# Kernel optimization log

Measured on AMD Instinct MI355X. Metric: run time of the kernel, lower is better.

The kernel has to match this reference:

```python
import jax, jax.numpy as jnp
import numpy as np

B, L, H, Q = 64, 512, 1024, 64
VA_H = 256


def setup_inputs() -> dict:
    key = jax.random.key(0)
    ks = jax.random.split(key, 10)
    hidden_states = jax.random.normal(ks[0], (B, L, H), dtype=jnp.float32)
    quad_spans = jax.random.randint(ks[1], (B, Q, 4), 0, L, dtype=jnp.int64)
    quad_mask = jnp.ones((B, Q), dtype=jnp.int32)
    s = 0.02
    W1 = jax.random.normal(ks[2], (3 * H, VA_H), dtype=jnp.float32) * s
    b1 = jnp.zeros((VA_H,), dtype=jnp.float32)
    W2 = jax.random.normal(ks[3], (VA_H, VA_H // 2), dtype=jnp.float32) * s
    b2 = jnp.zeros((VA_H // 2,), dtype=jnp.float32)
    W3 = jax.random.normal(ks[4], (VA_H // 2, 2), dtype=jnp.float32) * s
    b3 = jnp.zeros((2,), dtype=jnp.float32)
    return {"hidden_states": hidden_states, "quad_spans": quad_spans,
            "quad_mask": quad_mask, "W1": W1, "b1": b1, "W2": W2, "b2": b2,
            "W3": W3, "b3": b3}


def _pool_spans(hidden_states, quad_spans, quad_mask):
    # hidden_states [B,L,H]; quad_spans [B,Q,4]; quad_mask [B,Q]
    Bn, Ln, Hn = hidden_states.shape
    pos = jnp.arange(Ln)[None, None, :]                      # [1,1,L]
    asp_s = quad_spans[:, :, 0:1]
    asp_e = quad_spans[:, :, 1:2]
    opi_s = quad_spans[:, :, 2:3]
    opi_e = quad_spans[:, :, 3:4]
    asp_valid = asp_s >= 2
    opi_valid = opi_s >= 2
    sep = pos == 1                                           # [SEP] fallback
    asp_m = ((pos >= asp_s) & (pos <= asp_e) & asp_valid) | (~asp_valid & sep)
    opi_m = ((pos >= opi_s) & (pos <= opi_e) & opi_valid) | (~opi_valid & sep)
    qm = (quad_mask != 0)[:, :, None]
    asp_f = (asp_m & qm).astype(hidden_states.dtype)         # [B,Q,L]
    opi_f = (opi_m & qm).astype(hidden_states.dtype)
    h_asp = jnp.einsum('bql,blh->bqh', asp_f, hidden_states) / jnp.clip(
        asp_f.sum(-1, keepdims=True), 1.0, None)
    h_opi = jnp.einsum('bql,blh->bqh', opi_f, hidden_states) / jnp.clip(
        opi_f.sum(-1, keepdims=True), 1.0, None)
    return h_asp, h_opi


def reference(hidden_states, quad_spans, quad_mask, W1, b1, W2, b2, W3, b3):
    h_asp, h_opi = _pool_spans(hidden_states, quad_spans, quad_mask)
    h_pair = jnp.concatenate([h_asp, h_opi, h_asp * h_opi], axis=-1)  # [B,Q,3H]
    x = jax.nn.gelu(h_pair @ W1 + b1, approximate=False)   # torch GELU = exact
    x = jax.nn.gelu(x @ W2 + b2, approximate=False)        # dropout: eval mode
    x = x @ W3 + b3                                        # [B,Q,2]
    va = jax.nn.sigmoid(x) * 8.0 + 1.0
    return va * quad_mask[:, :, None].astype(va.dtype)
```

## Files before the change

kernel.cpp:

```cpp
#include <hip/hip_runtime.h>
#include <math.h>


typedef __attribute__((ext_vector_type(4))) float f32x4;
typedef __attribute__((ext_vector_type(8))) short bf16x8;

#define NPAIR 4096
#define LSEQ 512
#define HDIM 1024

__device__ __forceinline__ unsigned short f2bf(float f) {
  unsigned int x = __float_as_uint(f);
  return (unsigned short)((x + 0x7fffu + ((x >> 16) & 1u)) >> 16);
}
__device__ __forceinline__ unsigned int pack2(float lo, float hi) {
  return (unsigned int)f2bf(lo) | ((unsigned int)f2bf(hi) << 16);
}

__global__ __launch_bounds__(256, 2) void pool_mfma_kernel(
    const float* __restrict__ hs, const int* __restrict__ spans,
    const int* __restrict__ qmask, unsigned short* __restrict__ hpair) {
  __shared__ __align__(16) unsigned short Bl[128][40];
  __shared__ float S[128][129];
  __shared__ float scl[128];

  const int b = blockIdx.x >> 3;
  const int n0 = (blockIdx.x & 7) * 128;
  const int tid = threadIdx.x;
  const int lane = tid & 63;
  const int lm = lane & 15, quad = lane >> 4;
  const int wm = (tid >> 6) * 32;

  const bool is64 =
      (spans[1] == 0) && (spans[3] == 0) && (spans[5] == 0) && (spans[7] == 0);

  auto span_of = [&](int r, int& s, int& e) {
    const int q = r & 63, t = r >> 6;
    const int idx = (b * 64 + q) * 4 + t * 2;
    s = is64 ? spans[idx * 2] : spans[idx];
    e = is64 ? spans[idx * 2 + 2] : spans[idx + 1];
    if (s < 2) { s = 1; e = 1; }
  };
  int s0, e0, s1, e1;
  span_of(wm + lm, s0, e0);
  span_of(wm + 16 + lm, s1, e1);

  if (tid < 128) {
    int s, e;
    span_of(tid, s, e);
    const int c = (e >= s) ? (e - s + 1) : 0;
    const float sc = 1.f / (float)(c < 1 ? 1 : c);
    scl[tid] = (qmask[b * 64 + (tid & 63)] != 0) ? sc : 0.f;
  }

  f32x4 acc[2][8];
#pragma unroll
  for (int f = 0; f < 2; ++f)
#pragma unroll
    for (int g = 0; g < 8; ++g) acc[f][g] = f32x4{0.f, 0.f, 0.f, 0.f};

  const float* hsb = hs + (size_t)b * (LSEQ * HDIM);
  const int nl = tid & 127;
  const int kb = (tid >> 7) * 16;

  for (int k0 = 0; k0 < LSEQ; k0 += 32) {
    const float* src = hsb + (size_t)(k0 + kb) * HDIM + n0 + nl;
    unsigned int tmp[8];
#pragma unroll
    for (int i = 0; i < 8; ++i) {
      const float f0 = src[(size_t)(2 * i) * HDIM];
      const float f1 = src[(size_t)(2 * i + 1) * HDIM];
      tmp[i] = pack2(f0, f1);
    }
    __syncthreads();
    *(uint4*)&Bl[nl][kb] = make_uint4(tmp[0], tmp[1], tmp[2], tmp[3]);
    *(uint4*)&Bl[nl][kb + 8] = make_uint4(tmp[4], tmp[5], tmp[6], tmp[7]);
    __syncthreads();

    bf16x8 a0, a1;
#pragma unroll
    for (int j = 0; j < 8; ++j) {
      const int k = k0 + quad * 8 + j;
      a0[j] = (short)((k >= s0 && k <= e0) ? 0x3F80 : 0);
      a1[j] = (short)((k >= s1 && k <= e1) ? 0x3F80 : 0);
    }
#pragma unroll
    for (int g = 0; g < 8; ++g) {
      bf16x8 bg = *(const bf16x8*)&Bl[g * 16 + lm][quad * 8];
      acc[0][g] = __builtin_amdgcn_mfma_f32_16x16x32_bf16(a0, bg, acc[0][g], 0, 0, 0);
      acc[1][g] = __builtin_amdgcn_mfma_f32_16x16x32_bf16(a1, bg, acc[1][g], 0, 0, 0);
    }
  }

#pragma unroll
  for (int f = 0; f < 2; ++f)
#pragma unroll
    for (int g = 0; g < 8; ++g)
#pragma unroll
      for (int r = 0; r < 4; ++r)
        S[wm + f * 16 + quad * 4 + r][g * 16 + lm] = acc[f][g][r];
  __syncthreads();

  const int q = tid >> 2;
  const int cg = (tid & 3) * 32;
  const float sA = scl[q], sO = scl[64 + q];
  unsigned short* dst = hpair + (size_t)(b * 64 + q) * 3072 + n0 + cg;
#pragma unroll
  for (int j4 = 0; j4 < 4; ++j4) {
    float a[8], o[8];
#pragma unroll
    for (int i = 0; i < 8; ++i) {
      a[i] = S[q][cg + j4 * 8 + i] * sA;
      o[i] = S[64 + q][cg + j4 * 8 + i] * sO;
    }
    uint4 wa, wo, wp;
    wa.x = pack2(a[0], a[1]); wa.y = pack2(a[2], a[3]);
    wa.z = pack2(a[4], a[5]); wa.w = pack2(a[6], a[7]);
    wo.x = pack2(o[0], o[1]); wo.y = pack2(o[2], o[3]);
    wo.z = pack2(o[4], o[5]); wo.w = pack2(o[6], o[7]);
    wp.x = pack2(a[0] * o[0], a[1] * o[1]); wp.y = pack2(a[2] * o[2], a[3] * o[3]);
    wp.z = pack2(a[4] * o[4], a[5] * o[5]); wp.w = pack2(a[6] * o[6], a[7] * o[7]);
    *(uint4*)(dst + j4 * 8) = wa;
    *(uint4*)(dst + 1024 + j4 * 8) = wo;
    *(uint4*)(dst + 2048 + j4 * 8) = wp;
  }
}

__global__ void transpose_f32_bf16(const float* __restrict__ in,
                                   unsigned short* __restrict__ out, int R,
                                   int C) {
  __shared__ float t[32][33];
  const int c0 = blockIdx.x * 32, r0 = blockIdx.y * 32;
  const int x = threadIdx.x, y = threadIdx.y;
#pragma unroll
  for (int i = 0; i < 32; i += 8)
    if (r0 + y + i < R && c0 + x < C)
      t[y + i][x] = in[(size_t)(r0 + y + i) * C + c0 + x];
  __syncthreads();
#pragma unroll
  for (int i = 0; i < 32; i += 8)
    if (c0 + y + i < C && r0 + x < R)
      out[(size_t)(c0 + y + i) * R + r0 + x] = f2bf(t[x][y + i]);
}

template <int ACT>
__global__ __launch_bounds__(256) void gemm_bt_bias_act(
    const unsigned short* __restrict__ A, const unsigned short* __restrict__ Bt,
    const float* __restrict__ bias, unsigned short* __restrict__ C, int M,
    int N, int K) {
  __shared__ __align__(16) unsigned short Al[64][40];
  __shared__ __align__(16) unsigned short Bl[64][40];
  const int bm = blockIdx.x * 64, bn = blockIdx.y * 64;
  const int tid = threadIdx.x;
  const int wave = tid >> 6, lane = tid & 63;
  const int wm = (wave & 1) * 32, wn = (wave >> 1) * 32;
  const int ar = tid >> 2, ac = (tid & 3) * 8;
  const int lm = lane & 15, lk = (lane >> 4) * 8;

  f32x4 acc00 = {0.f, 0.f, 0.f, 0.f}, acc01 = {0.f, 0.f, 0.f, 0.f};
  f32x4 acc10 = {0.f, 0.f, 0.f, 0.f}, acc11 = {0.f, 0.f, 0.f, 0.f};

  const unsigned short* pa = A + (size_t)(bm + ar) * K + ac;
  const unsigned short* pb = Bt + (size_t)(bn + ar) * K + ac;

  for (int k0 = 0; k0 < K; k0 += 32) {
    uint4 va = *(const uint4*)(pa + k0);
    uint4 vb = *(const uint4*)(pb + k0);
    *(uint4*)&Al[ar][ac] = va;
    *(uint4*)&Bl[ar][ac] = vb;
    __syncthreads();
    bf16x8 a0 = *(const bf16x8*)&Al[wm + lm][lk];
    bf16x8 a1 = *(const bf16x8*)&Al[wm + 16 + lm][lk];
    bf16x8 b0 = *(const bf16x8*)&Bl[wn + lm][lk];
    bf16x8 b1 = *(const bf16x8*)&Bl[wn + 16 + lm][lk];
    acc00 = __builtin_amdgcn_mfma_f32_16x16x32_bf16(a0, b0, acc00, 0, 0, 0);
    acc01 = __builtin_amdgcn_mfma_f32_16x16x32_bf16(a0, b1, acc01, 0, 0, 0);
    acc10 = __builtin_amdgcn_mfma_f32_16x16x32_bf16(a1, b0, acc10, 0, 0, 0);
    acc11 = __builtin_amdgcn_mfma_f32_16x16x32_bf16(a1, b1, acc11, 0, 0, 0);
    __syncthreads();
  }

  const int r0 = bm + wm + ((lane >> 4) << 2);
  const int c0 = bn + wn + lm;
  const float bs0 = bias[c0];
  const float bs1 = bias[c0 + 16];
  auto emit = [&](f32x4 v, int row0, int col, float bs) {
#pragma unroll
    for (int r = 0; r < 4; ++r) {
      float x = v[r] + bs;
      if (ACT == 1) x = 0.5f * x * (1.f + erff(x * 0.70710678118654752f));
      C[(size_t)(row0 + r) * N + col] = f2bf(x);
    }
  };
  emit(acc00, r0, c0, bs0);
  emit(acc10, r0 + 16, c0, bs0);
  emit(acc01, r0, c0 + 16, bs1);
  emit(acc11, r0 + 16, c0 + 16, bs1);
}

__global__ __launch_bounds__(256) void head_kernel(
    const unsigned short* __restrict__ x2, const float* __restrict__ W3,
    const float* __restrict__ b3, const int* __restrict__ qmask,
    float* __restrict__ out) {
  __shared__ float w3[256];
  const int tid = threadIdx.x;
  w3[tid] = W3[tid];
  __syncthreads();
  const int p = blockIdx.x * 256 + tid;
  float acc0 = b3[0];
  float acc1 = b3[1];
  const uint4* xr = (const uint4*)(x2 + (size_t)p * 128);
#pragma unroll
  for (int kk = 0; kk < 16; ++kk) {
    uint4 v = xr[kk];
    const int k = kk * 8;
    float x0 = __uint_as_float((v.x & 0xffffu) << 16);
    float x1 = __uint_as_float((v.x >> 16) << 16);
    float x2e = __uint_as_float((v.y & 0xffffu) << 16);
    float x3 = __uint_as_float((v.y >> 16) << 16);
    float x4 = __uint_as_float((v.z & 0xffffu) << 16);
    float x5 = __uint_as_float((v.z >> 16) << 16);
    float x6 = __uint_as_float((v.w & 0xffffu) << 16);
    float x7 = __uint_as_float((v.w >> 16) << 16);
    acc0 += x0 * w3[2 * k + 0];  acc1 += x0 * w3[2 * k + 1];
    acc0 += x1 * w3[2 * k + 2];  acc1 += x1 * w3[2 * k + 3];
    acc0 += x2e * w3[2 * k + 4]; acc1 += x2e * w3[2 * k + 5];
    acc0 += x3 * w3[2 * k + 6];  acc1 += x3 * w3[2 * k + 7];
    acc0 += x4 * w3[2 * k + 8];  acc1 += x4 * w3[2 * k + 9];
    acc0 += x5 * w3[2 * k + 10]; acc1 += x5 * w3[2 * k + 11];
    acc0 += x6 * w3[2 * k + 12]; acc1 += x6 * w3[2 * k + 13];
    acc0 += x7 * w3[2 * k + 14]; acc1 += x7 * w3[2 * k + 15];
  }
  const float qmf = (float)qmask[p];
  const float v0 = (1.f / (1.f + expf(-acc0))) * 8.f + 1.f;
  const float v1 = (1.f / (1.f + expf(-acc1))) * 8.f + 1.f;
  out[p * 2 + 0] = v0 * qmf;
  out[p * 2 + 1] = v1 * qmf;
}

extern "C" void kernel_launch(void* const* d_in, const int* in_sizes, int n_in,
                              void* d_out, int out_size, void* d_ws,
                              size_t ws_size, hipStream_t stream) {
  const float* hs = (const float*)d_in[0];
  const int* spans = (const int*)d_in[1];
  const int* qmask = (const int*)d_in[2];
  const float* W1 = (const float*)d_in[3];
  const float* b1 = (const float*)d_in[4];
  const float* W2 = (const float*)d_in[5];
  const float* b2 = (const float*)d_in[6];
  const float* W3 = (const float*)d_in[7];
  const float* b3 = (const float*)d_in[8];
  float* out = (float*)d_out;

  const size_t HPAIR_B = 25165824;
  const size_t X1_B = 2097152, X2_B = 1048576;
  const size_t W1T_B = 1572864;

  char* ws = (char*)d_ws;
  size_t off = 0;
  unsigned short* hpair = (unsigned short*)(ws + off); off += HPAIR_B;
  unsigned short* x1 = (unsigned short*)(ws + off);    off += X1_B;
  unsigned short* x2 = (unsigned short*)(ws + off);    off += X2_B;
  unsigned short* W1T = (unsigned short*)(ws + off);   off += W1T_B;
  unsigned short* W2T = (unsigned short*)(ws + off);

  transpose_f32_bf16<<<dim3(8, 96), dim3(32, 8), 0, stream>>>(W1, W1T, 3072,
                                                              256);
  transpose_f32_bf16<<<dim3(4, 8), dim3(32, 8), 0, stream>>>(W2, W2T, 256,
                                                             128);
  pool_mfma_kernel<<<512, 256, 0, stream>>>(hs, spans, qmask, hpair);
  gemm_bt_bias_act<1><<<dim3(64, 4), 256, 0, stream>>>(hpair, W1T, b1, x1,
                                                       NPAIR, 256, 3072);
  gemm_bt_bias_act<1><<<dim3(64, 2), 256, 0, stream>>>(x1, W2T, b2, x2, NPAIR,
                                                       128, 256);
  head_kernel<<<16, 256, 0, stream>>>(x2, W3, b3, qmask, out);
}
```

Measured before the change: 267.4 us.

## Double-buffer pooling loads, split-K GEMM1, fuse GEMM2 with head, merge transposes

The pooling kernel now double-buffers its LDS tile, using a shared buffer that is reused for the output staging. This lets the global loads for the next K chunk overlap the MFMA work on the current one. GEMM1 is split along K into two halves to double the grid from 256 blocks, followed by a separate reduce+bias+GELU kernel. GEMM2 is fused with the final 128->2 head so x2 is no longer written out, and the two weight transposes are merged into one launch. The split-K path adds an extra fp32 partial-buffer round trip and one more kernel launch.

```diff
diff --git a/kernel.cpp b/kernel.cpp
--- a/kernel.cpp
+++ b/kernel.cpp
@@ -16,13 +16,18 @@
 __device__ __forceinline__ unsigned int pack2(float lo, float hi) {
   return (unsigned int)f2bf(lo) | ((unsigned int)f2bf(hi) << 16);
 }
+__device__ __forceinline__ float gelu(float x) {
+  return 0.5f * x * (1.f + erff(x * 0.70710678118654752f));
+}
 
 __global__ __launch_bounds__(256, 2) void pool_mfma_kernel(
     const float* __restrict__ hs, const int* __restrict__ spans,
     const int* __restrict__ qmask, unsigned short* __restrict__ hpair) {
-  __shared__ __align__(16) unsigned short Bl[128][40];
-  __shared__ float S[128][129];
+  __shared__ __align__(16) unsigned char smem[66048];
   __shared__ float scl[128];
+  typedef unsigned short BlT[128][40];
+  BlT* Bl = (BlT*)smem;
+  float(*S)[129] = (float(*)[129])smem;
 
   const int b = blockIdx.x >> 3;
   const int n0 = (blockIdx.x & 7) * 128;
@@ -63,19 +68,25 @@
   const int nl = tid & 127;
   const int kb = (tid >> 7) * 16;
 
-  for (int k0 = 0; k0 < LSEQ; k0 += 32) {
-    const float* src = hsb + (size_t)(k0 + kb) * HDIM + n0 + nl;
-    unsigned int tmp[8];
+  auto load16 = [&](int kbase, unsigned int (&tmp)[8]) {
+    const float* src = hsb + (size_t)(kbase + kb) * HDIM + n0 + nl;
 #pragma unroll
     for (int i = 0; i < 8; ++i) {
       const float f0 = src[(size_t)(2 * i) * HDIM];
       const float f1 = src[(size_t)(2 * i + 1) * HDIM];
       tmp[i] = pack2(f0, f1);
     }
-    __syncthreads();
-    *(uint4*)&Bl[nl][kb] = make_uint4(tmp[0], tmp[1], tmp[2], tmp[3]);
-    *(uint4*)&Bl[nl][kb + 8] = make_uint4(tmp[4], tmp[5], tmp[6], tmp[7]);
-    __syncthreads();
+  };
+
+  unsigned int tmp[8];
+  load16(0, tmp);
+  *(uint4*)&Bl[0][nl][kb] = make_uint4(tmp[0], tmp[1], tmp[2], tmp[3]);
+  *(uint4*)&Bl[0][nl][kb + 8] = make_uint4(tmp[4], tmp[5], tmp[6], tmp[7]);
+
+  for (int it = 0; it < 16; ++it) {
+    const int k0 = it * 32;
+    __syncthreads();
+    if (it < 15) load16(k0 + 32, tmp);
 
     bf16x8 a0, a1;
 #pragma unroll
@@ -84,14 +95,21 @@
       a0[j] = (short)((k >= s0 && k <= e0) ? 0x3F80 : 0);
       a1[j] = (short)((k >= s1 && k <= e1) ? 0x3F80 : 0);
     }
+    const BlT& Bc = Bl[it & 1];
 #pragma unroll
     for (int g = 0; g < 8; ++g) {
-      bf16x8 bg = *(const bf16x8*)&Bl[g * 16 + lm][quad * 8];
+      bf16x8 bg = *(const bf16x8*)&Bc[g * 16 + lm][quad * 8];
       acc[0][g] = __builtin_amdgcn_mfma_f32_16x16x32_bf16(a0, bg, acc[0][g], 0, 0, 0);
       acc[1][g] = __builtin_amdgcn_mfma_f32_16x16x32_bf16(a1, bg, acc[1][g], 0, 0, 0);
     }
-  }
-
+    if (it < 15) {
+      BlT& Bn = Bl[(it + 1) & 1];
+      *(uint4*)&Bn[nl][kb] = make_uint4(tmp[0], tmp[1], tmp[2], tmp[3]);
+      *(uint4*)&Bn[nl][kb + 8] = make_uint4(tmp[4], tmp[5], tmp[6], tmp[7]);
+    }
+  }
+
+  __syncthreads();
 #pragma unroll
   for (int f = 0; f < 2; ++f)
 #pragma unroll
@@ -126,31 +144,40 @@
   }
 }
 
-__global__ void transpose_f32_bf16(const float* __restrict__ in,
-                                   unsigned short* __restrict__ out, int R,
-                                   int C) {
+__global__ void transpose_two(const float* __restrict__ W1,
+                              unsigned short* __restrict__ W1T,
+                              const float* __restrict__ W2,
+                              unsigned short* __restrict__ W2T) {
   __shared__ float t[32][33];
-  const int c0 = blockIdx.x * 32, r0 = blockIdx.y * 32;
+  const float* in;
+  unsigned short* out;
+  int R, C, c0, r0;
+  int blk = blockIdx.x;
+  if (blk < 768) {
+    in = W1; out = W1T; R = 3072; C = 256;
+    c0 = (blk & 7) * 32; r0 = (blk >> 3) * 32;
+  } else {
+    blk -= 768;
+    in = W2; out = W2T; R = 256; C = 128;
+    c0 = (blk & 3) * 32; r0 = (blk >> 2) * 32;
+  }
   const int x = threadIdx.x, y = threadIdx.y;
 #pragma unroll
   for (int i = 0; i < 32; i += 8)
-    if (r0 + y + i < R && c0 + x < C)
-      t[y + i][x] = in[(size_t)(r0 + y + i) * C + c0 + x];
+    t[y + i][x] = in[(size_t)(r0 + y + i) * C + c0 + x];
   __syncthreads();
 #pragma unroll
   for (int i = 0; i < 32; i += 8)
-    if (c0 + y + i < C && r0 + x < R)
-      out[(size_t)(c0 + y + i) * R + r0 + x] = f2bf(t[x][y + i]);
-}
-
-template <int ACT>
-__global__ __launch_bounds__(256) void gemm_bt_bias_act(
+    out[(size_t)(c0 + y + i) * R + r0 + x] = f2bf(t[x][y + i]);
+}
+
+__global__ __launch_bounds__(256) void gemm_bt_partial(
     const unsigned short* __restrict__ A, const unsigned short* __restrict__ Bt,
-    const float* __restrict__ bias, unsigned short* __restrict__ C, int M,
-    int N, int K) {
+    float* __restrict__ P, int M, int N, int K, int KH) {
   __shared__ __align__(16) unsigned short Al[64][40];
   __shared__ __align__(16) unsigned short Bl[64][40];
   const int bm = blockIdx.x * 64, bn = blockIdx.y * 64;
+  const int kz = blockIdx.z * KH;
   const int tid = threadIdx.x;
   const int wave = tid >> 6, lane = tid & 63;
   const int wm = (wave & 1) * 32, wn = (wave >> 1) * 32;
@@ -160,10 +187,10 @@
   f32x4 acc00 = {0.f, 0.f, 0.f, 0.f}, acc01 = {0.f, 0.f, 0.f, 0.f};
   f32x4 acc10 = {0.f, 0.f, 0.f, 0.f}, acc11 = {0.f, 0.f, 0.f, 0.f};
 
-  const unsigned short* pa = A + (size_t)(bm + ar) * K + ac;
-  const unsigned short* pb = Bt + (size_t)(bn + ar) * K + ac;
-
-  for (int k0 = 0; k0 < K; k0 += 32) {
+  const unsigned short* pa = A + (size_t)(bm + ar) * K + kz + ac;
+  const unsigned short* pb = Bt + (size_t)(bn + ar) * K + kz + ac;
+
+  for (int k0 = 0; k0 < KH; k0 += 32) {
     uint4 va = *(const uint4*)(pa + k0);
     uint4 vb = *(const uint4*)(pb + k0);
     *(uint4*)&Al[ar][ac] = va;
@@ -180,62 +207,107 @@
     __syncthreads();
   }
 
+  float* Pz = P + (size_t)blockIdx.z * M * N;
   const int r0 = bm + wm + ((lane >> 4) << 2);
   const int c0 = bn + wn + lm;
-  const float bs0 = bias[c0];
-  const float bs1 = bias[c0 + 16];
-  auto emit = [&](f32x4 v, int row0, int col, float bs) {
-#pragma unroll
-    for (int r = 0; r < 4; ++r) {
-      float x = v[r] + bs;
-      if (ACT == 1) x = 0.5f * x * (1.f + erff(x * 0.70710678118654752f));
-      C[(size_t)(row0 + r) * N + col] = f2bf(x);
-    }
+  auto emit = [&](f32x4 v, int row0, int col) {
+#pragma unroll
+    for (int r = 0; r < 4; ++r) Pz[(size_t)(row0 + r) * N + col] = v[r];
   };
-  emit(acc00, r0, c0, bs0);
-  emit(acc10, r0 + 16, c0, bs0);
-  emit(acc01, r0, c0 + 16, bs1);
-  emit(acc11, r0 + 16, c0 + 16, bs1);
-}
-
-__global__ __launch_bounds__(256) void head_kernel(
-    const unsigned short* __restrict__ x2, const float* __restrict__ W3,
+  emit(acc00, r0, c0);
+  emit(acc10, r0 + 16, c0);
+  emit(acc01, r0, c0 + 16);
+  emit(acc11, r0 + 16, c0 + 16);
+}
+
+__global__ __launch_bounds__(256) void reduce_bias_gelu(
+    const float* __restrict__ P, const float* __restrict__ bias,
+    unsigned short* __restrict__ X) {
+  const int t = blockIdx.x * 256 + threadIdx.x;
+  const int e = t * 4;
+  float4 p0 = *(const float4*)(P + e);
+  float4 p1 = *(const float4*)(P + (size_t)NPAIR * 256 + e);
+  float4 bs = *(const float4*)(bias + (e & 255));
+  const float v0 = gelu(p0.x + p1.x + bs.x);
+  const float v1 = gelu(p0.y + p1.y + bs.y);
+  const float v2 = gelu(p0.z + p1.z + bs.z);
+  const float v3 = gelu(p0.w + p1.w + bs.w);
+  uint2 w;
+  w.x = pack2(v0, v1);
+  w.y = pack2(v2, v3);
+  *(uint2*)(X + e) = w;
+}
+
+__global__ __launch_bounds__(256) void gemm2_head_kernel(
+    const unsigned short* __restrict__ A, const unsigned short* __restrict__ Bt,
+    const float* __restrict__ b2, const float* __restrict__ W3,
     const float* __restrict__ b3, const int* __restrict__ qmask,
     float* __restrict__ out) {
+  __shared__ __align__(16) unsigned short Al[64][40];
+  __shared__ __align__(16) unsigned short Bl[128][40];
+  __shared__ float S2[64][129];
   __shared__ float w3[256];
+
+  const int bm = blockIdx.x * 64;
   const int tid = threadIdx.x;
+  const int wave = tid >> 6, lane = tid & 63;
+  const int wm = (wave & 1) * 32, wn = (wave >> 1) * 64;
+  const int ar = tid >> 2, ac = (tid & 3) * 8;
+  const int br = tid >> 1, bc = (tid & 1) * 16;
+  const int lm = lane & 15, quad = lane >> 4;
+
   w3[tid] = W3[tid];
+
+  f32x4 acc[2][4];
+#pragma unroll
+  for (int f = 0; f < 2; ++f)
+#pragma unroll
+    for (int g = 0; g < 4; ++g) acc[f][g] = f32x4{0.f, 0.f, 0.f, 0.f};
+
+  const unsigned short* pa = A + (size_t)(bm + ar) * 256 + ac;
+  const unsigned short* pb = Bt + (size_t)br * 256 + bc;
+
+  for (int k0 = 0; k0 < 256; k0 += 32) {
+    uint4 va = *(const uint4*)(pa + k0);
+    uint4 vb0 = *(const uint4*)(pb + k0);
+    uint4 vb1 = *(const uint4*)(pb + k0 + 8);
+    *(uint4*)&Al[ar][ac] = va;
+    *(uint4*)&Bl[br][bc] = vb0;
+    *(uint4*)&Bl[br][bc + 8] = vb1;
+    __syncthreads();
+    bf16x8 a0 = *(const bf16x8*)&Al[wm + lm][quad * 8];
+    bf16x8 a1 = *(const bf16x8*)&Al[wm + 16 + lm][quad * 8];
+#pragma unroll
+    for (int g = 0; g < 4; ++g) {
+      bf16x8 bg = *(const bf16x8*)&Bl[wn + g * 16 + lm][quad * 8];
+      acc[0][g] = __builtin_amdgcn_mfma_f32_16x16x32_bf16(a0, bg, acc[0][g], 0, 0, 0);
+      acc[1][g] = __builtin_amdgcn_mfma_f32_16x16x32_bf16(a1, bg, acc[1][g], 0, 0, 0);
+    }
+    __syncthreads();
+  }
+
+#pragma unroll
+  for (int f = 0; f < 2; ++f)
+#pragma unroll
+    for (int g = 0; g < 4; ++g) {
+      const int col = wn + g * 16 + lm;
+#pragma unroll
+      for (int r = 0; r < 4; ++r) {
+        const int row = wm + f * 16 + quad * 4 + r;
+        S2[row][col] = gelu(acc[f][g][r] + b2[col]);
+      }
+    }
   __syncthreads();
-  const int p = blockIdx.x * 256 + tid;
-  float acc0 = b3[0];
-  float acc1 = b3[1];
-  const uint4* xr = (const uint4*)(x2 + (size_t)p * 128);
-#pragma unroll
-  for (int kk = 0; kk < 16; ++kk) {
-    uint4 v = xr[kk];
-    const int k = kk * 8;
-    float x0 = __uint_as_float((v.x & 0xffffu) << 16);
-    float x1 = __uint_as_float((v.x >> 16) << 16);
-    float x2e = __uint_as_float((v.y & 0xffffu) << 16);
-    float x3 = __uint_as_float((v.y >> 16) << 16);
-    float x4 = __uint_as_float((v.z & 0xffffu) << 16);
-    float x5 = __uint_as_float((v.z >> 16) << 16);
-    float x6 = __uint_as_float((v.w & 0xffffu) << 16);
-    float x7 = __uint_as_float((v.w >> 16) << 16);
-    acc0 += x0 * w3[2 * k + 0];  acc1 += x0 * w3[2 * k + 1];
-    acc0 += x1 * w3[2 * k + 2];  acc1 += x1 * w3[2 * k + 3];
-    acc0 += x2e * w3[2 * k + 4]; acc1 += x2e * w3[2 * k + 5];
-    acc0 += x3 * w3[2 * k + 6];  acc1 += x3 * w3[2 * k + 7];
-    acc0 += x4 * w3[2 * k + 8];  acc1 += x4 * w3[2 * k + 9];
-    acc0 += x5 * w3[2 * k + 10]; acc1 += x5 * w3[2 * k + 11];
-    acc0 += x6 * w3[2 * k + 12]; acc1 += x6 * w3[2 * k + 13];
-    acc0 += x7 * w3[2 * k + 14]; acc1 += x7 * w3[2 * k + 15];
-  }
-  const float qmf = (float)qmask[p];
-  const float v0 = (1.f / (1.f + expf(-acc0))) * 8.f + 1.f;
-  const float v1 = (1.f / (1.f + expf(-acc1))) * 8.f + 1.f;
-  out[p * 2 + 0] = v0 * qmf;
-  out[p * 2 + 1] = v1 * qmf;
+
+  if (tid < 128) {
+    const int row = tid >> 1, o = tid & 1;
+    float a = b3[o];
+#pragma unroll 8
+    for (int c = 0; c < 128; ++c) a += S2[row][c] * w3[c * 2 + o];
+    const int pair = bm + row;
+    const float qmf = (float)qmask[pair];
+    out[pair * 2 + o] = ((1.f / (1.f + expf(-a))) * 8.f + 1.f) * qmf;
+  }
 }
 
 extern "C" void kernel_launch(void* const* d_in, const int* in_sizes, int n_in,
@@ -253,25 +325,22 @@
   float* out = (float*)d_out;
 
   const size_t HPAIR_B = 25165824;
-  const size_t X1_B = 2097152, X2_B = 1048576;
+  const size_t X1_B = 2097152;
+  const size_t P_B = 2 * 4194304;
   const size_t W1T_B = 1572864;
 
   char* ws = (char*)d_ws;
   size_t off = 0;
   unsigned short* hpair = (unsigned short*)(ws + off); off += HPAIR_B;
   unsigned short* x1 = (unsigned short*)(ws + off);    off += X1_B;
-  unsigned short* x2 = (unsigned short*)(ws + off);    off += X2_B;
+  float* P = (float*)(ws + off);                       off += P_B;
   unsigned short* W1T = (unsigned short*)(ws + off);   off += W1T_B;
   unsigned short* W2T = (unsigned short*)(ws + off);
 
-  transpose_f32_bf16<<<dim3(8, 96), dim3(32, 8), 0, stream>>>(W1, W1T, 3072,
-                                                              256);
-  transpose_f32_bf16<<<dim3(4, 8), dim3(32, 8), 0, stream>>>(W2, W2T, 256,
-                                                             128);
+  transpose_two<<<800, dim3(32, 8), 0, stream>>>(W1, W1T, W2, W2T);
   pool_mfma_kernel<<<512, 256, 0, stream>>>(hs, spans, qmask, hpair);
-  gemm_bt_bias_act<1><<<dim3(64, 4), 256, 0, stream>>>(hpair, W1T, b1, x1,
-                                                       NPAIR, 256, 3072);
-  gemm_bt_bias_act<1><<<dim3(64, 2), 256, 0, stream>>>(x1, W2T, b2, x2, NPAIR,
-                                                       128, 256);
-  head_kernel<<<16, 256, 0, stream>>>(x2, W3, b3, qmask, out);
-}
+  gemm_bt_partial<<<dim3(64, 4, 2), 256, 0, stream>>>(hpair, W1T, P, NPAIR,
+                                                      256, 3072, 1536);
+  reduce_bias_gelu<<<1024, 256, 0, stream>>>(P, b1, x1);
+  gemm2_head_kernel<<<64, 256, 0, stream>>>(x1, W2T, b2, W3, b3, qmask, out);
+}
```

Measured after the change: 250.8 us. 1.07x faster.
